# Kernel optimization log

Measured on AMD Instinct MI355X. Metric: run time of the kernel, lower is better.

The kernel has to match this reference:

```python
import jax, jax.numpy as jnp
import numpy as np

N, E, B = 50000, 300000, 8
XD, ED, H, L, G = 160, 16, 256, 4, 32


def setup_inputs() -> dict:
    key = jax.random.key(0)
    ks = jax.random.split(key, 24)
    w = lambda k, shape: jax.random.normal(k, shape, jnp.float32) * 0.05
    z = lambda *shape: jnp.zeros(shape, jnp.float32)
    in_dim = G + (XD - 128)
    return {
        "x": jax.random.normal(ks[0], (N, XD), jnp.float32),
        "edge_attr": jax.random.normal(ks[1], (E, ED), jnp.float32),
        "geo_w": w(ks[2], (128, G)), "geo_b": z(G),
        "nin_w1": w(ks[3], (in_dim, H)), "nin_b1": z(H),
        "nin_w2": w(ks[4], (H, H)), "nin_b2": z(H),
        "ee_w1": w(ks[5], (ED, H)), "ee_b1": z(H),
        "ee_w2": w(ks[6], (H, H)), "ee_b2": z(H),
        "msgx_w": w(ks[7], (L, H, H)),
        "msge_w": w(ks[8], (L, H, H)),
        "upd_w1": w(ks[9], (L, H, H)), "upd_b1": z(L, H),
        "upd_w2": w(ks[10], (L, H, H)), "upd_b2": z(L, H),
        "ln_g": jnp.ones((L, H), jnp.float32), "ln_b": z(L, H),
        "edge_index": jax.random.randint(ks[11], (2, E), 0, N),
        "batch": jnp.sort(jax.random.randint(ks[12], (N,), 0, B)),
        "node_type": jax.random.randint(ks[13], (N,), 0, 3),
    }


def _layernorm(v, g, b, eps=1e-5):
    mu = v.mean(-1, keepdims=True)
    var = ((v - mu) ** 2).mean(-1, keepdims=True)
    return (v - mu) / jnp.sqrt(var + eps) * g + b


def reference(x, edge_attr, geo_w, geo_b, nin_w1, nin_b1, nin_w2, nin_b2,
              ee_w1, ee_b1, ee_w2, ee_b2, msgx_w, msge_w,
              upd_w1, upd_b1, upd_w2, upd_b2, ln_g, ln_b,
              edge_index, batch, node_type):
    # geo projection of leading 128 dims, concat with remaining features
    geo = jax.nn.relu(x[:, :128] @ geo_w + geo_b)
    xin = jnp.concatenate([geo, x[:, 128:]], axis=1)
    # node_in MLP
    h = jax.nn.relu(xin @ nin_w1 + nin_b1) @ nin_w2 + nin_b2  # [N, H]
    # edge encoder MLP
    e = jax.nn.relu(edge_attr @ ee_w1 + ee_b1) @ ee_w2 + ee_b2  # [E, H]
    src, dst = edge_index[0], edge_index[1]
    for l in range(L):
        # message: msg_x(x_j) + msg_e(e), scatter-add to target nodes
        m = h[src] @ msgx_w[l] + e @ msge_w[l]  # [E, H]
        agg = jax.ops.segment_sum(m, dst, num_segments=N)  # [N, H]
        u = jax.nn.relu(agg @ upd_w1[l] + upd_b1[l]) @ upd_w2[l] + upd_b2[l]
        h = _layernorm(h + u, ln_g[l], ln_b[l])
    # masked mean-pool per graph for each node type
    def pool(k):
        mask = (node_type == k).astype(h.dtype)[:, None]  # [N, 1]
        s = jax.ops.segment_sum(h * mask, batch, num_segments=B)
        c = jax.ops.segment_sum(mask, batch, num_segments=B)
        return s / jnp.maximum(c, 1.0)
    z = jnp.concatenate([pool(0), pool(1), pool(2)], axis=1)  # [B, 3H]
    return (z, h, batch)
```

## Files before the change

kernel.cpp:

```cpp
#include <hip/hip_runtime.h>

constexpr int N  = 50000;
constexpr int E  = 300000;
constexpr int B  = 8;
constexpr int XD = 160;
constexpr int ED = 16;
constexpr int H  = 256;
constexpr int L  = 4;
constexpr int G  = 32;

typedef __attribute__((ext_vector_type(8))) short short8;
typedef __attribute__((ext_vector_type(4))) short sv4;
typedef __attribute__((ext_vector_type(4))) float floatx4;

__device__ __forceinline__ short f2bf(float f) {
    union { float f; unsigned u; } v; v.f = f;
    unsigned r = (v.u + 0x7fffu + ((v.u >> 16) & 1u)) >> 16;
    return (short)r;
}
__device__ __forceinline__ float bf2f(short s) {
    union { unsigned u; float f; } v;
    v.u = ((unsigned)(unsigned short)s) << 16;
    return v.f;
}

__global__ __launch_bounds__(256) void hist_kernel(
    const int* __restrict__ dst, int* __restrict__ cnt)
{
    int e = blockIdx.x * 256 + threadIdx.x;
    if (e < E) atomicAdd(&cnt[dst[e]], 1);
}

__global__ __launch_bounds__(256) void scan_partial_kernel(
    const int* __restrict__ cnt, int* __restrict__ bsum)
{
    __shared__ int s[256];
    const int tid = threadIdx.x;
    int i = blockIdx.x * 256 + tid;
    s[tid] = (i < N) ? cnt[i] : 0;
    __syncthreads();
    #pragma unroll
    for (int off = 128; off > 0; off >>= 1) {
        if (tid < off) s[tid] += s[tid + off];
        __syncthreads();
    }
    if (tid == 0) bsum[blockIdx.x] = s[0];
}

__global__ __launch_bounds__(256) void scan_bsum_kernel(
    int* __restrict__ bsum, int nb, int* __restrict__ rsN)
{
    __shared__ int s[256];
    const int tid = threadIdx.x;
    int v = (tid < nb) ? bsum[tid] : 0;
    s[tid] = v;
    __syncthreads();
    #pragma unroll
    for (int off = 1; off < 256; off <<= 1) {
        int x = (tid >= off) ? s[tid - off] : 0;
        __syncthreads();
        s[tid] += x;
        __syncthreads();
    }
    if (tid < nb) bsum[tid] = s[tid] - v;
    if (tid == 255) *rsN = s[255];
}

__global__ __launch_bounds__(256) void scan_final_kernel(
    const int* __restrict__ cnt, const int* __restrict__ bsum,
    int* __restrict__ rs, int* __restrict__ cursor)
{
    __shared__ int s[256];
    const int tid = threadIdx.x;
    int i = blockIdx.x * 256 + tid;
    int v = (i < N) ? cnt[i] : 0;
    s[tid] = v;
    __syncthreads();
    #pragma unroll
    for (int off = 1; off < 256; off <<= 1) {
        int x = (tid >= off) ? s[tid - off] : 0;
        __syncthreads();
        s[tid] += x;
        __syncthreads();
    }
    int excl = s[tid] - v + bsum[blockIdx.x];
    if (i < N) { rs[i] = excl; cursor[i] = excl; }
}

__global__ __launch_bounds__(256) void fill_kernel(
    const int* __restrict__ src, const int* __restrict__ dst,
    int* __restrict__ cursor, int* __restrict__ csr_src, int* __restrict__ csr_eid)
{
    int e = blockIdx.x * 256 + threadIdx.x;
    if (e < E) {
        int d = dst[e];
        int pos = atomicAdd(&cursor[d], 1);
        csr_src[pos] = src[e];
        csr_eid[pos] = e;
    }
}

__global__ __launch_bounds__(256) void hidden_agg_kernel(
    const float* __restrict__ ea, const float* __restrict__ ew1,
    const float* __restrict__ eb1,
    const int* __restrict__ rs, const int* __restrict__ csr_eid,
    short* __restrict__ haggB)
{
    const int lane = threadIdx.x & 63;
    const int wave = threadIdx.x >> 6;
    const int n = blockIdx.x * 4 + wave;
    if (n >= N) return;

    float4 w[ED];
    #pragma unroll
    for (int k = 0; k < ED; ++k)
        w[k] = *(const float4*)&ew1[k * H + 4 * lane];
    float4 bb = *(const float4*)&eb1[4 * lane];

    const int s = rs[n], e = rs[n + 1];
    float4 acc = {0.f, 0.f, 0.f, 0.f};
    int j = s;
    for (; j + 1 < e; j += 2) {
        int e0 = csr_eid[j], e1 = csr_eid[j + 1];
        const float* a0 = ea + (size_t)e0 * ED;
        const float* a1 = ea + (size_t)e1 * ED;
        float4 h0 = bb, h1 = bb;
        #pragma unroll
        for (int k = 0; k < ED; ++k) {
            float v0 = a0[k], v1 = a1[k];
            h0.x += v0 * w[k].x; h1.x += v1 * w[k].x;
            h0.y += v0 * w[k].y; h1.y += v1 * w[k].y;
            h0.z += v0 * w[k].z; h1.z += v1 * w[k].z;
            h0.w += v0 * w[k].w; h1.w += v1 * w[k].w;
        }
        acc.x += fmaxf(h0.x, 0.f) + fmaxf(h1.x, 0.f);
        acc.y += fmaxf(h0.y, 0.f) + fmaxf(h1.y, 0.f);
        acc.z += fmaxf(h0.z, 0.f) + fmaxf(h1.z, 0.f);
        acc.w += fmaxf(h0.w, 0.f) + fmaxf(h1.w, 0.f);
    }
    if (j < e) {
        int e0 = csr_eid[j];
        const float* a0 = ea + (size_t)e0 * ED;
        float4 h0 = bb;
        #pragma unroll
        for (int k = 0; k < ED; ++k) {
            float v0 = a0[k];
            h0.x += v0 * w[k].x; h0.y += v0 * w[k].y;
            h0.z += v0 * w[k].z; h0.w += v0 * w[k].w;
        }
        acc.x += fmaxf(h0.x, 0.f); acc.y += fmaxf(h0.y, 0.f);
        acc.z += fmaxf(h0.z, 0.f); acc.w += fmaxf(h0.w, 0.f);
    }
    sv4 o = {f2bf(acc.x), f2bf(acc.y), f2bf(acc.z), f2bf(acc.w)};
    *(sv4*)&haggB[(size_t)n * H + 4 * lane] = o;
}

__global__ __launch_bounds__(256) void gather_kernel(
    const short* __restrict__ h_in_bf,
    const int* __restrict__ rs, const int* __restrict__ csr_src,
    short* __restrict__ agg_bf)
{
    const int lane = threadIdx.x & 63;
    const int wave = threadIdx.x >> 6;
    const int n = blockIdx.x * 4 + wave;
    if (n >= N) return;
    const int s = rs[n], e = rs[n + 1];
    float4 acc = {0.f, 0.f, 0.f, 0.f};
    int j = s;
    for (; j + 4 <= e; j += 4) {
        const int s0 = csr_src[j],     s1 = csr_src[j + 1];
        const int s2 = csr_src[j + 2], s3 = csr_src[j + 3];
        sv4 v0 = *(const sv4*)&h_in_bf[(size_t)s0 * H + 4 * lane];
        sv4 v1 = *(const sv4*)&h_in_bf[(size_t)s1 * H + 4 * lane];
        sv4 v2 = *(const sv4*)&h_in_bf[(size_t)s2 * H + 4 * lane];
        sv4 v3 = *(const sv4*)&h_in_bf[(size_t)s3 * H + 4 * lane];
        acc.x += (bf2f(v0.x) + bf2f(v1.x)) + (bf2f(v2.x) + bf2f(v3.x));
        acc.y += (bf2f(v0.y) + bf2f(v1.y)) + (bf2f(v2.y) + bf2f(v3.y));
        acc.z += (bf2f(v0.z) + bf2f(v1.z)) + (bf2f(v2.z) + bf2f(v3.z));
        acc.w += (bf2f(v0.w) + bf2f(v1.w)) + (bf2f(v2.w) + bf2f(v3.w));
    }
    for (; j < e; ++j) {
        const int s0 = csr_src[j];
        sv4 v0 = *(const sv4*)&h_in_bf[(size_t)s0 * H + 4 * lane];
        acc.x += bf2f(v0.x); acc.y += bf2f(v0.y);
        acc.z += bf2f(v0.z); acc.w += bf2f(v0.w);
    }
    sv4 o = {f2bf(acc.x), f2bf(acc.y), f2bf(acc.z), f2bf(acc.w)};
    *(sv4*)&agg_bf[(size_t)n * H + 4 * lane] = o;
}

__global__ __launch_bounds__(256) void wx_part_kernel(
    const float* __restrict__ msgx_w, short* __restrict__ wxwe)
{
    int l = blockIdx.x >> 8, k = blockIdx.x & 255, n = threadIdx.x;
    wxwe[((size_t)(l * H + n)) * 512 + k] = f2bf(msgx_w[((size_t)l * H + k) * H + n]);
}

__global__ __launch_bounds__(256) void we_fuse_kernel(
    const float* __restrict__ ee_w2, const float* __restrict__ msge_w,
    short* __restrict__ wxwe)
{
    __shared__ float wrow[H];
    const int tid = threadIdx.x;
    const int l = blockIdx.x / H;
    const int t = blockIdx.x % H;
    wrow[tid] = ee_w2[t * H + tid];
    __syncthreads();
    const float* mw = msge_w + (size_t)l * H * H;
    float acc = 0.f;
    for (int k = 0; k < H; ++k)
        acc += wrow[k] * mw[k * H + tid];
    wxwe[((size_t)(l * H + tid)) * 512 + 256 + t] = f2bf(acc);
}

__global__ __launch_bounds__(256) void fuse_b_kernel(
    const float* __restrict__ ee_b2, const float* __restrict__ msge_w,
    float* __restrict__ be2)
{
    __shared__ float brow[H];
    const int tid = threadIdx.x;
    const int l = blockIdx.x;
    brow[tid] = ee_b2[tid];
    __syncthreads();
    const float* mw = msge_w + (size_t)l * H * H;
    float acc = 0.f;
    for (int k = 0; k < H; ++k)
        acc += brow[k] * mw[k * H + tid];
    be2[l * H + tid] = acc;
}

__global__ __launch_bounds__(256) void conv_bt_kernel(
    const float* __restrict__ w, short* __restrict__ bt)
{
    int mat = blockIdx.x >> 8, k = blockIdx.x & 255, n = threadIdx.x;
    bt[((size_t)mat * H + n) * H + k] = f2bf(w[((size_t)mat * H + k) * H + n]);
}

__global__ __launch_bounds__(256) void geow_bt_kernel(
    const float* __restrict__ w, short* __restrict__ bt)
{
    for (int i = threadIdx.x; i < 32 * 128; i += 256) {
        int n = i >> 7, k = i & 127;
        bt[i] = f2bf(w[k * 32 + n]);
    }
}

__global__ __launch_bounds__(256) void ninw1_bt_kernel(
    const float* __restrict__ w, short* __restrict__ bt)
{
    int i = blockIdx.x * 256 + threadIdx.x;
    int n = i >> 6, k = i & 63;
    bt[i] = f2bf(w[k * H + n]);
}

__global__ __launch_bounds__(256) void node_in_mfma_kernel(
    const float* __restrict__ x,
    const short* __restrict__ geo_wbt, const float* __restrict__ geo_b,
    const short* __restrict__ w1bt, const float* __restrict__ b1,
    const short* __restrict__ w2bt, const float* __restrict__ b2,
    short* __restrict__ h_bf)
{
    constexpr int KP = H + 8;
    constexpr int KX = 128 + 8;
    constexpr int KI = 64 + 8;
    __shared__ short A[64 * KP];
    __shared__ short XIN[64 * KI];
    const int tid = threadIdx.x;
    const int lane = tid & 63, wave = tid >> 6;
    const int quad = lane >> 4, lm = lane & 15;
    const int n0 = blockIdx.x * 64;
    const int nvalid = min(64, N - n0);
    const int ncol = wave * 64 + lm;

    for (int i = tid; i < 64 * 128; i += 256) {
        int row = i >> 7, k = i & 127;
        float v = (row < nvalid) ? x[(size_t)(n0 + row) * XD + k] : 0.f;
        A[row * KX + k] = f2bf(v);
    }
    for (int i = tid; i < 64 * 32; i += 256) {
        int row = i >> 5, k = i & 31;
        float v = (row < nvalid) ? x[(size_t)(n0 + row) * XD + 128 + k] : 0.f;
        XIN[row * KI + 32 + k] = f2bf(v);
    }
    __syncthreads();

    {
        floatx4 c[2];
        float b0 = geo_b[lm], b1v = geo_b[16 + lm];
        c[0] = {b0, b0, b0, b0};
        c[1] = {b1v, b1v, b1v, b1v};
        #pragma unroll
        for (int ks = 0; ks < 4; ++ks) {
            short8 a  = *(const short8*)&A[(wave * 16 + lm) * KX + ks * 32 + quad * 8];
            short8 w0 = *(const short8*)&geo_wbt[(size_t)lm * 128 + ks * 32 + quad * 8];
            short8 w1 = *(const short8*)&geo_wbt[(size_t)(16 + lm) * 128 + ks * 32 + quad * 8];
            c[0] = __builtin_amdgcn_mfma_f32_16x16x32_bf16(a, w0, c[0], 0, 0, 0);
            c[1] = __builtin_amdgcn_mfma_f32_16x16x32_bf16(a, w1, c[1], 0, 0, 0);
        }
        #pragma unroll
        for (int nt = 0; nt < 2; ++nt)
            #pragma unroll
            for (int r = 0; r < 4; ++r) {
                int row = wave * 16 + quad * 4 + r;
                XIN[row * KI + nt * 16 + lm] = f2bf(fmaxf(c[nt][r], 0.f));
            }
    }
    __syncthreads();

    floatx4 c1[4][4];
    #pragma unroll
    for (int nt = 0; nt < 4; ++nt) {
        float bb = b1[ncol + nt * 16];
        #pragma unroll
        for (int mt = 0; mt < 4; ++mt) {
            c1[mt][nt][0] = bb; c1[mt][nt][1] = bb;
            c1[mt][nt][2] = bb; c1[mt][nt][3] = bb;
        }
    }
    #pragma unroll
    for (int ks = 0; ks < 2; ++ks) {
        short8 a[4], b[4];
        #pragma unroll
        for (int mt = 0; mt < 4; ++mt)
            a[mt] = *(const short8*)&XIN[(mt * 16 + lm) * KI + ks * 32 + quad * 8];
        #pragma unroll
        for (int nt = 0; nt < 4; ++nt)
            b[nt] = *(const short8*)&w1bt[(size_t)(ncol + nt * 16) * 64 + ks * 32 + quad * 8];
        #pragma unroll
        for (int mt = 0; mt < 4; ++mt)
            #pragma unroll
            for (int nt = 0; nt < 4; ++nt)
                c1[mt][nt] = __builtin_amdgcn_mfma_f32_16x16x32_bf16(a[mt], b[nt], c1[mt][nt], 0, 0, 0);
    }
    __syncthreads();
    #pragma unroll
    for (int mt = 0; mt < 4; ++mt)
        #pragma unroll
        for (int nt = 0; nt < 4; ++nt) {
            int col = ncol + nt * 16;
            #pragma unroll
            for (int r = 0; r < 4; ++r) {
                int row = mt * 16 + quad * 4 + r;
                A[row * KP + col] = f2bf(fmaxf(c1[mt][nt][r], 0.f));
            }
        }
    __syncthreads();

    floatx4 c2[4][4];
    #pragma unroll
    for (int nt = 0; nt < 4; ++nt) {
        float bb = b2[ncol + nt * 16];
        #pragma unroll
        for (int mt = 0; mt < 4; ++mt) {
            c2[mt][nt][0] = bb; c2[mt][nt][1] = bb;
            c2[mt][nt][2] = bb; c2[mt][nt][3] = bb;
        }
    }
    #pragma unroll
    for (int ks = 0; ks < 8; ++ks) {
        short8 a[4], b[4];
        #pragma unroll
        for (int mt = 0; mt < 4; ++mt)
            a[mt] = *(const short8*)&A[(mt * 16 + lm) * KP + ks * 32 + quad * 8];
        #pragma unroll
        for (int nt = 0; nt < 4; ++nt)
            b[nt] = *(const short8*)&w2bt[(size_t)(ncol + nt * 16) * H + ks * 32 + quad * 8];
        #pragma unroll
        for (int mt = 0; mt < 4; ++mt)
            #pragma unroll
            for (int nt = 0; nt < 4; ++nt)
                c2[mt][nt] = __builtin_amdgcn_mfma_f32_16x16x32_bf16(a[mt], b[nt], c2[mt][nt], 0, 0, 0);
    }
    #pragma unroll
    for (int mt = 0; mt < 4; ++mt)
        #pragma unroll
        for (int r = 0; r < 4; ++r) {
            int row = mt * 16 + quad * 4 + r;
            if (row < nvalid) {
                #pragma unroll
                for (int nt = 0; nt < 4; ++nt)
                    h_bf[(size_t)(n0 + row) * H + ncol + nt * 16] = f2bf(c2[mt][nt][r]);
            }
        }
}

__global__ __launch_bounds__(256, 4) void layer_kernel(
    const short* __restrict__ h_in_bf, short* __restrict__ h_out_bf,
    float* __restrict__ h_out_f32,
    const short* __restrict__ agg_bf,
    const int* __restrict__ rs,
    const short* __restrict__ haggB,
    const short* __restrict__ wxwe, const float* __restrict__ be2,
    const short* __restrict__ u1bt, const float* __restrict__ b1,
    const short* __restrict__ u2bt, const float* __restrict__ b2,
    const float* __restrict__ lng, const float* __restrict__ lnb)
{
    constexpr int KP = H + 8;
    constexpr int M  = 32;
    __shared__ short A[M * KP];
    __shared__ short A2[M * KP];
    __shared__ int rsL[M + 1];
    __shared__ float psum[M][4], psq[M][4];
    __shared__ float muS[M], rsS[M];
    const int tid  = threadIdx.x;
    const int lane = tid & 63, wave = tid >> 6;
    const int quad = lane >> 4, lm = lane & 15;
    const int n0 = blockIdx.x * M;
    const int nvalid = min(M, N - n0);
    const int ncol = wave * 64 + lm;

    if (tid < M + 1) rsL[tid] = rs[min(n0 + tid, N)];
    for (int i = tid; i < M * 64; i += 256) {
        int row = i >> 6, q = i & 63;
        sv4 v = {0, 0, 0, 0};
        sv4 w = {0, 0, 0, 0};
        if (row < nvalid) {
            v = *(const sv4*)&agg_bf[(size_t)(n0 + row) * H + 4 * q];
            w = *(const sv4*)&haggB[(size_t)(n0 + row) * H + 4 * q];
        }
        *(sv4*)&A[row * KP + 4 * q]  = v;
        *(sv4*)&A2[row * KP + 4 * q] = w;
    }
    __syncthreads();

    floatx4 c1[2][4];
    #pragma unroll
    for (int nt = 0; nt < 4; ++nt) {
        float bb = be2[ncol + nt * 16];
        #pragma unroll
        for (int mt = 0; mt < 2; ++mt) {
            #pragma unroll
            for (int r = 0; r < 4; ++r) {
                int row = mt * 16 + quad * 4 + r;
                float deg = (float)(rsL[row + 1] - rsL[row]);
                c1[mt][nt][r] = deg * bb;
            }
        }
    }
    {
        short8 bcur[4], bnxt[4];
        #pragma unroll
        for (int nt = 0; nt < 4; ++nt)
            bcur[nt] = *(const short8*)&wxwe[(size_t)(ncol + nt * 16) * 512 + quad * 8];
        #pragma unroll
        for (int ks = 0; ks < 8; ++ks) {
            if (ks < 7) {
                #pragma unroll
                for (int nt = 0; nt < 4; ++nt)
                    bnxt[nt] = *(const short8*)&wxwe[(size_t)(ncol + nt * 16) * 512 + (ks + 1) * 32 + quad * 8];
            }
            short8 a[2];
            #pragma unroll
            for (int mt = 0; mt < 2; ++mt)
                a[mt] = *(const short8*)&A[(mt * 16 + lm) * KP + ks * 32 + quad * 8];
            #pragma unroll
            for (int mt = 0; mt < 2; ++mt)
                #pragma unroll
                for (int nt = 0; nt < 4; ++nt)
                    c1[mt][nt] = __builtin_amdgcn_mfma_f32_16x16x32_bf16(a[mt], bcur[nt], c1[mt][nt], 0, 0, 0);
            #pragma unroll
            for (int nt = 0; nt < 4; ++nt) bcur[nt] = bnxt[nt];
        }
    }
    {
        short8 bcur[4], bnxt[4];
        #pragma unroll
        for (int nt = 0; nt < 4; ++nt)
            bcur[nt] = *(const short8*)&wxwe[(size_t)(ncol + nt * 16) * 512 + 256 + quad * 8];
        #pragma unroll
        for (int ks = 0; ks < 8; ++ks) {
            if (ks < 7) {
                #pragma unroll
                for (int nt = 0; nt < 4; ++nt)
                    bnxt[nt] = *(const short8*)&wxwe[(size_t)(ncol + nt * 16) * 512 + 256 + (ks + 1) * 32 + quad * 8];
            }
            short8 a[2];
            #pragma unroll
            for (int mt = 0; mt < 2; ++mt)
                a[mt] = *(const short8*)&A2[(mt * 16 + lm) * KP + ks * 32 + quad * 8];
            #pragma unroll
            for (int mt = 0; mt < 2; ++mt)
                #pragma unroll
                for (int nt = 0; nt < 4; ++nt)
                    c1[mt][nt] = __builtin_amdgcn_mfma_f32_16x16x32_bf16(a[mt], bcur[nt], c1[mt][nt], 0, 0, 0);
            #pragma unroll
            for (int nt = 0; nt < 4; ++nt) bcur[nt] = bnxt[nt];
        }
    }
    __syncthreads();
    #pragma unroll
    for (int mt = 0; mt < 2; ++mt)
        #pragma unroll
        for (int nt = 0; nt < 4; ++nt) {
            int col = ncol + nt * 16;
            #pragma unroll
            for (int r = 0; r < 4; ++r) {
                int row = mt * 16 + quad * 4 + r;
                A[row * KP + col] = f2bf(c1[mt][nt][r]);
            }
        }
    __syncthreads();

    floatx4 c2[2][4];
    #pragma unroll
    for (int nt = 0; nt < 4; ++nt) {
        float bb = b1[ncol + nt * 16];
        #pragma unroll
        for (int mt = 0; mt < 2; ++mt) {
            c2[mt][nt][0] = bb; c2[mt][nt][1] = bb;
            c2[mt][nt][2] = bb; c2[mt][nt][3] = bb;
        }
    }
    {
        short8 bcur[4], bnxt[4];
        #pragma unroll
        for (int nt = 0; nt < 4; ++nt)
            bcur[nt] = *(const short8*)&u1bt[(size_t)(ncol + nt * 16) * H + quad * 8];
        #pragma unroll
        for (int ks = 0; ks < 8; ++ks) {
            if (ks < 7) {
                #pragma unroll
                for (int nt = 0; nt < 4; ++nt)
                    bnxt[nt] = *(const short8*)&u1bt[(size_t)(ncol + nt * 16) * H + (ks + 1) * 32 + quad * 8];
            }
            short8 a[2];
            #pragma unroll
            for (int mt = 0; mt < 2; ++mt)
                a[mt] = *(const short8*)&A[(mt * 16 + lm) * KP + ks * 32 + quad * 8];
            #pragma unroll
            for (int mt = 0; mt < 2; ++mt)
                #pragma unroll
                for (int nt = 0; nt < 4; ++nt)
                    c2[mt][nt] = __builtin_amdgcn_mfma_f32_16x16x32_bf16(a[mt], bcur[nt], c2[mt][nt], 0, 0, 0);
            #pragma unroll
            for (int nt = 0; nt < 4; ++nt) bcur[nt] = bnxt[nt];
        }
    }
    #pragma unroll
    for (int mt = 0; mt < 2; ++mt)
        #pragma unroll
        for (int nt = 0; nt < 4; ++nt) {
            int col = ncol + nt * 16;
            #pragma unroll
            for (int r = 0; r < 4; ++r) {
                int row = mt * 16 + quad * 4 + r;
                A2[row * KP + col] = f2bf(fmaxf(c2[mt][nt][r], 0.f));
            }
        }
    __syncthreads();

    floatx4 c3[2][4];
    #pragma unroll
    for (int nt = 0; nt < 4; ++nt) {
        float bb = b2[ncol + nt * 16];
        #pragma unroll
        for (int mt = 0; mt < 2; ++mt) {
            c3[mt][nt][0] = bb; c3[mt][nt][1] = bb;
            c3[mt][nt][2] = bb; c3[mt][nt][3] = bb;
        }
    }
    {
        short8 bcur[4], bnxt[4];
        #pragma unroll
        for (int nt = 0; nt < 4; ++nt)
            bcur[nt] = *(const short8*)&u2bt[(size_t)(ncol + nt * 16) * H + quad * 8];
        #pragma unroll
        for (int ks = 0; ks < 8; ++ks) {
            if (ks < 7) {
                #pragma unroll
                for (int nt = 0; nt < 4; ++nt)
                    bnxt[nt] = *(const short8*)&u2bt[(size_t)(ncol + nt * 16) * H + (ks + 1) * 32 + quad * 8];
            }
            short8 a[2];
            #pragma unroll
            for (int mt = 0; mt < 2; ++mt)
                a[mt] = *(const short8*)&A2[(mt * 16 + lm) * KP + ks * 32 + quad * 8];
            #pragma unroll
            for (int mt = 0; mt < 2; ++mt)
                #pragma unroll
                for (int nt = 0; nt < 4; ++nt)
                    c3[mt][nt] = __builtin_amdgcn_mfma_f32_16x16x32_bf16(a[mt], bcur[nt], c3[mt][nt], 0, 0, 0);
            #pragma unroll
            for (int nt = 0; nt < 4; ++nt) bcur[nt] = bnxt[nt];
        }
    }
    #pragma unroll
    for (int mt = 0; mt < 2; ++mt)
        #pragma unroll
        for (int r = 0; r < 4; ++r) {
            int row = mt * 16 + quad * 4 + r;
            if (row < nvalid) {
                #pragma unroll
                for (int nt = 0; nt < 4; ++nt)
                    c3[mt][nt][r] += bf2f(h_in_bf[(size_t)(n0 + row) * H + ncol + nt * 16]);
            }
        }

    #pragma unroll
    for (int mt = 0; mt < 2; ++mt)
        #pragma unroll
        for (int r = 0; r < 4; ++r) {
            float s = 0.f, q = 0.f;
            #pragma unroll
            for (int nt = 0; nt < 4; ++nt) {
                float v = c3[mt][nt][r];
                s += v; q += v * v;
            }
            #pragma unroll
            for (int m = 1; m < 16; m <<= 1) {
                s += __shfl_xor(s, m, 64);
                q += __shfl_xor(q, m, 64);
            }
            if (lm == 0) {
                int row = mt * 16 + quad * 4 + r;
                psum[row][wave] = s;
                psq[row][wave]  = q;
            }
        }
    __syncthreads();
    if (tid < M) {
        float s = psum[tid][0] + psum[tid][1] + psum[tid][2] + psum[tid][3];
        float q = psq[tid][0] + psq[tid][1] + psq[tid][2] + psq[tid][3];
        float mu = s * (1.f / H);
        float var = q * (1.f / H) - mu * mu;
        muS[tid] = mu;
        rsS[tid] = rsqrtf(fmaxf(var, 0.f) + 1e-5f);
    }
    __syncthreads();

    float g[4], bb4[4];
    #pragma unroll
    for (int nt = 0; nt < 4; ++nt) {
        g[nt]   = lng[ncol + nt * 16];
        bb4[nt] = lnb[ncol + nt * 16];
    }
    const bool wbf = (h_out_bf != nullptr);
    const bool wf  = (h_out_f32 != nullptr);
    #pragma unroll
    for (int mt = 0; mt < 2; ++mt)
        #pragma unroll
        for (int r = 0; r < 4; ++r) {
            int row = mt * 16 + quad * 4 + r;
            if (row < nvalid) {
                float mu = muS[row], rsv = rsS[row];
                #pragma unroll
                for (int nt = 0; nt < 4; ++nt) {
                    float o = (c3[mt][nt][r] - mu) * rsv * g[nt] + bb4[nt];
                    size_t off = (size_t)(n0 + row) * H + ncol + nt * 16;
                    if (wbf) h_out_bf[off] = f2bf(o);
                    if (wf)  h_out_f32[off] = o;
                }
            }
        }
}

__global__ __launch_bounds__(256) void pool_kernel(
    const float* __restrict__ h, const int* __restrict__ batch,
    const int* __restrict__ ntype,
    float* __restrict__ zsum, float* __restrict__ zcnt)
{
    constexpr int CHUNK = 256;
    __shared__ float acc[3][H];
    __shared__ float cnt[3];
    const int tid = threadIdx.x;
    const int n0 = blockIdx.x * CHUNK;
    const int nend = min(n0 + CHUNK, N);

    for (int q = 0; q < 3; ++q) acc[q][tid] = 0.f;
    if (tid == 0) { cnt[0] = 0.f; cnt[1] = 0.f; cnt[2] = 0.f; }
    __syncthreads();

    int cur = batch[n0];
    for (int n = n0; n < nend; ++n) {
        int b = batch[n];
        int t = ntype[n];
        if (b != cur) {
            for (int q = 0; q < 3; ++q) {
                atomicAdd(&zsum[cur * (3 * H) + q * H + tid], acc[q][tid]);
                acc[q][tid] = 0.f;
            }
            if (tid == 0)
                for (int q = 0; q < 3; ++q) { atomicAdd(&zcnt[cur * 3 + q], cnt[q]); cnt[q] = 0.f; }
            cur = b;
        }
        acc[t][tid] += h[(size_t)n * H + tid];
        if (tid == 0) cnt[t] += 1.f;
    }
    for (int q = 0; q < 3; ++q)
        atomicAdd(&zsum[cur * (3 * H) + q * H + tid], acc[q][tid]);
    if (tid == 0)
        for (int q = 0; q < 3; ++q) atomicAdd(&zcnt[cur * 3 + q], cnt[q]);
}

__global__ __launch_bounds__(256) void finalize_kernel(
    const float* __restrict__ zsum, const float* __restrict__ zcnt,
    float* __restrict__ out)
{
    int idx = blockIdx.x * 256 + threadIdx.x;
    if (idx >= B * 3 * H) return;
    int b = idx / (3 * H);
    int c = idx % (3 * H);
    int t = c / H;
    float cn = zcnt[b * 3 + t];
    out[idx] = zsum[idx] / fmaxf(cn, 1.f);
}

__global__ __launch_bounds__(256) void batch_out_kernel(
    const int* __restrict__ batch, float* __restrict__ out)
{
    int idx = blockIdx.x * 256 + threadIdx.x;
    if (idx < N) out[idx] = (float)batch[idx];
}

extern "C" void kernel_launch(void* const* d_in, const int* in_sizes, int n_in,
                              void* d_out, int out_size, void* d_ws, size_t ws_size,
                              hipStream_t stream) {
    const float* x         = (const float*)d_in[0];
    const float* edge_attr = (const float*)d_in[1];
    const float* geo_w     = (const float*)d_in[2];
    const float* geo_b     = (const float*)d_in[3];
    const float* nin_w1    = (const float*)d_in[4];
    const float* nin_b1    = (const float*)d_in[5];
    const float* nin_w2    = (const float*)d_in[6];
    const float* nin_b2    = (const float*)d_in[7];
    const float* ee_w1     = (const float*)d_in[8];
    const float* ee_b1     = (const float*)d_in[9];
    const float* ee_w2     = (const float*)d_in[10];
    const float* ee_b2     = (const float*)d_in[11];
    const float* msgx_w    = (const float*)d_in[12];
    const float* msge_w    = (const float*)d_in[13];
    const float* upd_w1    = (const float*)d_in[14];
    const float* upd_b1    = (const float*)d_in[15];
    const float* upd_w2    = (const float*)d_in[16];
    const float* upd_b2    = (const float*)d_in[17];
    const float* ln_g      = (const float*)d_in[18];
    const float* ln_b      = (const float*)d_in[19];
    const int*   edge_index= (const int*)d_in[20];
    const int*   batch     = (const int*)d_in[21];
    const int*   node_type = (const int*)d_in[22];

    float* out = (float*)d_out;
    float* hf  = out + B * 3 * H;

    short* h0_bf   = (short*)d_ws;
    short* h1_bf   = h0_bf + (size_t)N * H;
    short* haggB   = h1_bf + (size_t)N * H;
    short* wxwe    = haggB + (size_t)N * H;
    short* u1bt    = wxwe + (size_t)L * H * 512;
    short* u2bt    = u1bt + (size_t)L * H * H;
    short* geowbt  = u2bt + (size_t)L * H * H;
    short* w1bt    = geowbt + 32 * 128;
    short* w2bt    = w1bt + H * 64;
    float* be2     = (float*)(w2bt + H * H);
    float* zsum    = be2 + L * H;
    float* zcnt    = zsum + B * 3 * H;
    int*   rowcnt  = (int*)(zcnt + B * 3);
    int*   rs      = rowcnt + N;
    int*   cursor  = rs + N + 1;
    int*   bsum    = cursor + N;
    int*   csr_src = bsum + 256;
    int*   csr_eid = csr_src + E;

    const int* src = edge_index;
    const int* dst = edge_index + E;

    const int nscan = (N + 255) / 256;

    hipMemsetAsync(rowcnt, 0, (size_t)N * sizeof(int), stream);
    hist_kernel<<<(E + 255) / 256, 256, 0, stream>>>(dst, rowcnt);
    scan_partial_kernel<<<nscan, 256, 0, stream>>>(rowcnt, bsum);
    scan_bsum_kernel<<<1, 256, 0, stream>>>(bsum, nscan, rs + N);
    scan_final_kernel<<<nscan, 256, 0, stream>>>(rowcnt, bsum, rs, cursor);
    fill_kernel<<<(E + 255) / 256, 256, 0, stream>>>(src, dst, cursor, csr_src, csr_eid);

    wx_part_kernel<<<L * 256, 256, 0, stream>>>(msgx_w, wxwe);
    we_fuse_kernel<<<L * H, 256, 0, stream>>>(ee_w2, msge_w, wxwe);
    fuse_b_kernel<<<L, 256, 0, stream>>>(ee_b2, msge_w, be2);
    conv_bt_kernel<<<L * 256, 256, 0, stream>>>(upd_w1, u1bt);
    conv_bt_kernel<<<L * 256, 256, 0, stream>>>(upd_w2, u2bt);
    conv_bt_kernel<<<256, 256, 0, stream>>>(nin_w2, w2bt);
    geow_bt_kernel<<<1, 256, 0, stream>>>(geo_w, geowbt);
    ninw1_bt_kernel<<<64, 256, 0, stream>>>(nin_w1, w1bt);

    hidden_agg_kernel<<<(N + 3) / 4, 256, 0, stream>>>(
        edge_attr, ee_w1, ee_b1, rs, csr_eid, haggB);

    node_in_mfma_kernel<<<(N + 63) / 64, 256, 0, stream>>>(
        x, geowbt, geo_b, w1bt, nin_b1, w2bt, nin_b2, h0_bf);

    const int lgrid = (N + 31) / 32;
    for (int l = 0; l < L; ++l) {
        const short* hin  = (l & 1) ? h1_bf : h0_bf;
        short* aggb       = (l & 1) ? h0_bf : h1_bf;
        short* hout_bf    = (l == L - 1) ? nullptr : aggb;
        float* hout_f32   = (l == L - 1) ? hf : nullptr;
        gather_kernel<<<(N + 3) / 4, 256, 0, stream>>>(hin, rs, csr_src, aggb);
        layer_kernel<<<lgrid, 256, 0, stream>>>(
            hin, hout_bf, hout_f32, aggb, rs, haggB,
            wxwe + (size_t)l * H * 512, be2 + (size_t)l * H,
            u1bt + (size_t)l * H * H, upd_b1 + (size_t)l * H,
            u2bt + (size_t)l * H * H, upd_b2 + (size_t)l * H,
            ln_g + (size_t)l * H, ln_b + (size_t)l * H);
    }

    hipMemsetAsync(zsum, 0, (size_t)(B * 3 * H + B * 3) * sizeof(float), stream);
    pool_kernel<<<(N + 255) / 256, 256, 0, stream>>>(hf, batch, node_type, zsum, zcnt);
    finalize_kernel<<<(B * 3 * H + 255) / 256, 256, 0, stream>>>(zsum, zcnt, out);
    batch_out_kernel<<<(N + 255) / 256, 256, 0, stream>>>(batch, out + B * 3 * H + (size_t)N * H);
}
```

Measured before the change: 1.050 ms.

## Fold upd_w1 into message weights to drop one GEMM per layer

Since agg feeds linearly into upd_w1 before the ReLU, the message weights (msgx_w and fused ee_w2·msge_w) are premultiplied by upd_w1 in fp32 at setup, and the bias becomes deg·(be2·W1)+b1. The layer kernel then runs one K=512 GEMM straight into the ReLU instead of the message GEMM plus a separate 256x256 update GEMM, removing an LDS round trip and a sync. This adds setup kernels computing the weight products and changes bf16 rounding points, since the intermediate agg result is no longer quantised.

Measured after the change: 977.4 us. -6.9%, faster.

```diff
diff --git a/kernel.cpp b/kernel.cpp
--- a/kernel.cpp
+++ b/kernel.cpp
@@ -189,16 +189,9 @@
     *(sv4*)&agg_bf[(size_t)n * H + 4 * lane] = o;
 }
 
-__global__ __launch_bounds__(256) void wx_part_kernel(
-    const float* __restrict__ msgx_w, short* __restrict__ wxwe)
-{
-    int l = blockIdx.x >> 8, k = blockIdx.x & 255, n = threadIdx.x;
-    wxwe[((size_t)(l * H + n)) * 512 + k] = f2bf(msgx_w[((size_t)l * H + k) * H + n]);
-}
-
 __global__ __launch_bounds__(256) void we_fuse_kernel(
     const float* __restrict__ ee_w2, const float* __restrict__ msge_w,
-    short* __restrict__ wxwe)
+    float* __restrict__ WEf32)
 {
     __shared__ float wrow[H];
     const int tid = threadIdx.x;
@@ -210,7 +203,41 @@
     float acc = 0.f;
     for (int k = 0; k < H; ++k)
         acc += wrow[k] * mw[k * H + tid];
-    wxwe[((size_t)(l * H + tid)) * 512 + 256 + t] = f2bf(acc);
+    WEf32[((size_t)l * H + t) * H + tid] = acc;
+}
+
+__global__ __launch_bounds__(256) void fuse1_kernel(
+    const float* __restrict__ msgx_w, const float* __restrict__ upd_w1,
+    short* __restrict__ fusedT)
+{
+    __shared__ float wrow[H];
+    const int tid = threadIdx.x;
+    const int l = blockIdx.x / H;
+    const int t = blockIdx.x % H;
+    wrow[tid] = msgx_w[((size_t)l * H + t) * H + tid];
+    __syncthreads();
+    const float* w1 = upd_w1 + (size_t)l * H * H;
+    float acc = 0.f;
+    for (int j = 0; j < H; ++j)
+        acc += wrow[j] * w1[j * H + tid];
+    fusedT[((size_t)(l * H + tid)) * 512 + t] = f2bf(acc);
+}
+
+__global__ __launch_bounds__(256) void fuse2_kernel(
+    const float* __restrict__ WEf32, const float* __restrict__ upd_w1,
+    short* __restrict__ fusedT)
+{
+    __shared__ float wrow[H];
+    const int tid = threadIdx.x;
+    const int l = blockIdx.x / H;
+    const int t = blockIdx.x % H;
+    wrow[tid] = WEf32[((size_t)l * H + t) * H + tid];
+    __syncthreads();
+    const float* w1 = upd_w1 + (size_t)l * H * H;
+    float acc = 0.f;
+    for (int j = 0; j < H; ++j)
+        acc += wrow[j] * w1[j * H + tid];
+    fusedT[((size_t)(l * H + tid)) * 512 + 256 + t] = f2bf(acc);
 }
 
 __global__ __launch_bounds__(256) void fuse_b_kernel(
@@ -227,6 +254,22 @@
     for (int k = 0; k < H; ++k)
         acc += brow[k] * mw[k * H + tid];
     be2[l * H + tid] = acc;
+}
+
+__global__ __launch_bounds__(256) void fuse_bias_kernel(
+    const float* __restrict__ be2, const float* __restrict__ upd_w1,
+    float* __restrict__ be2w1)
+{
+    __shared__ float brow[H];
+    const int tid = threadIdx.x;
+    const int l = blockIdx.x;
+    brow[tid] = be2[l * H + tid];
+    __syncthreads();
+    const float* w1 = upd_w1 + (size_t)l * H * H;
+    float acc = 0.f;
+    for (int j = 0; j < H; ++j)
+        acc += brow[j] * w1[j * H + tid];
+    be2w1[l * H + tid] = acc;
 }
 
 __global__ __launch_bounds__(256) void conv_bt_kernel(
@@ -390,8 +433,8 @@
     const short* __restrict__ agg_bf,
     const int* __restrict__ rs,
     const short* __restrict__ haggB,
-    const short* __restrict__ wxwe, const float* __restrict__ be2,
-    const short* __restrict__ u1bt, const float* __restrict__ b1,
+    const short* __restrict__ fusedT, const float* __restrict__ be2w1,
+    const float* __restrict__ b1,
     const short* __restrict__ u2bt, const float* __restrict__ b2,
     const float* __restrict__ lng, const float* __restrict__ lnb)
 {
@@ -426,14 +469,15 @@
     floatx4 c1[2][4];
     #pragma unroll
     for (int nt = 0; nt < 4; ++nt) {
-        float bb = be2[ncol + nt * 16];
+        float bw = be2w1[ncol + nt * 16];
+        float bb = b1[ncol + nt * 16];
         #pragma unroll
         for (int mt = 0; mt < 2; ++mt) {
             #pragma unroll
             for (int r = 0; r < 4; ++r) {
                 int row = mt * 16 + quad * 4 + r;
                 float deg = (float)(rsL[row + 1] - rsL[row]);
-                c1[mt][nt][r] = deg * bb;
+                c1[mt][nt][r] = deg * bw + bb;
             }
         }
     }
@@ -441,13 +485,13 @@
         short8 bcur[4], bnxt[4];
         #pragma unroll
         for (int nt = 0; nt < 4; ++nt)
-            bcur[nt] = *(const short8*)&wxwe[(size_t)(ncol + nt * 16) * 512 + quad * 8];
+            bcur[nt] = *(const short8*)&fusedT[(size_t)(ncol + nt * 16) * 512 + quad * 8];
         #pragma unroll
         for (int ks = 0; ks < 8; ++ks) {
             if (ks < 7) {
                 #pragma unroll
                 for (int nt = 0; nt < 4; ++nt)
-                    bnxt[nt] = *(const short8*)&wxwe[(size_t)(ncol + nt * 16) * 512 + (ks + 1) * 32 + quad * 8];
+                    bnxt[nt] = *(const short8*)&fusedT[(size_t)(ncol + nt * 16) * 512 + (ks + 1) * 32 + quad * 8];
             }
             short8 a[2];
             #pragma unroll
@@ -466,13 +510,13 @@
         short8 bcur[4], bnxt[4];
         #pragma unroll
         for (int nt = 0; nt < 4; ++nt)
-            bcur[nt] = *(const short8*)&wxwe[(size_t)(ncol + nt * 16) * 512 + 256 + quad * 8];
+            bcur[nt] = *(const short8*)&fusedT[(size_t)(ncol + nt * 16) * 512 + 256 + quad * 8];
         #pragma unroll
         for (int ks = 0; ks < 8; ++ks) {
             if (ks < 7) {
                 #pragma unroll
                 for (int nt = 0; nt < 4; ++nt)
-                    bnxt[nt] = *(const short8*)&wxwe[(size_t)(ncol + nt * 16) * 512 + 256 + (ks + 1) * 32 + quad * 8];
+                    bnxt[nt] = *(const short8*)&fusedT[(size_t)(ncol + nt * 16) * 512 + 256 + (ks + 1) * 32 + quad * 8];
             }
             short8 a[2];
             #pragma unroll
@@ -496,55 +540,7 @@
             #pragma unroll
             for (int r = 0; r < 4; ++r) {
                 int row = mt * 16 + quad * 4 + r;
-                A[row * KP + col] = f2bf(c1[mt][nt][r]);
-            }
-        }
-    __syncthreads();
-
-    floatx4 c2[2][4];
-    #pragma unroll
-    for (int nt = 0; nt < 4; ++nt) {
-        float bb = b1[ncol + nt * 16];
-        #pragma unroll
-        for (int mt = 0; mt < 2; ++mt) {
-            c2[mt][nt][0] = bb; c2[mt][nt][1] = bb;
-            c2[mt][nt][2] = bb; c2[mt][nt][3] = bb;
-        }
-    }
-    {
-        short8 bcur[4], bnxt[4];
-        #pragma unroll
-        for (int nt = 0; nt < 4; ++nt)
-            bcur[nt] = *(const short8*)&u1bt[(size_t)(ncol + nt * 16) * H + quad * 8];
-        #pragma unroll
-        for (int ks = 0; ks < 8; ++ks) {
-            if (ks < 7) {
-                #pragma unroll
-                for (int nt = 0; nt < 4; ++nt)
-                    bnxt[nt] = *(const short8*)&u1bt[(size_t)(ncol + nt * 16) * H + (ks + 1) * 32 + quad * 8];
-            }
-            short8 a[2];
-            #pragma unroll
-            for (int mt = 0; mt < 2; ++mt)
-                a[mt] = *(const short8*)&A[(mt * 16 + lm) * KP + ks * 32 + quad * 8];
-            #pragma unroll
-            for (int mt = 0; mt < 2; ++mt)
-                #pragma unroll
-                for (int nt = 0; nt < 4; ++nt)
-                    c2[mt][nt] = __builtin_amdgcn_mfma_f32_16x16x32_bf16(a[mt], bcur[nt], c2[mt][nt], 0, 0, 0);
-            #pragma unroll
-            for (int nt = 0; nt < 4; ++nt) bcur[nt] = bnxt[nt];
-        }
-    }
-    #pragma unroll
-    for (int mt = 0; mt < 2; ++mt)
-        #pragma unroll
-        for (int nt = 0; nt < 4; ++nt) {
-            int col = ncol + nt * 16;
-            #pragma unroll
-            for (int r = 0; r < 4; ++r) {
-                int row = mt * 16 + quad * 4 + r;
-                A2[row * KP + col] = f2bf(fmaxf(c2[mt][nt][r], 0.f));
+                A[row * KP + col] = f2bf(fmaxf(c1[mt][nt][r], 0.f));
             }
         }
     __syncthreads();
@@ -574,7 +570,7 @@
             short8 a[2];
             #pragma unroll
             for (int mt = 0; mt < 2; ++mt)
-                a[mt] = *(const short8*)&A2[(mt * 16 + lm) * KP + ks * 32 + quad * 8];
+                a[mt] = *(const short8*)&A[(mt * 16 + lm) * KP + ks * 32 + quad * 8];
             #pragma unroll
             for (int mt = 0; mt < 2; ++mt)
                 #pragma unroll
@@ -745,14 +741,15 @@
     short* h0_bf   = (short*)d_ws;
     short* h1_bf   = h0_bf + (size_t)N * H;
     short* haggB   = h1_bf + (size_t)N * H;
-    short* wxwe    = haggB + (size_t)N * H;
-    short* u1bt    = wxwe + (size_t)L * H * 512;
-    short* u2bt    = u1bt + (size_t)L * H * H;
+    short* fusedT  = haggB + (size_t)N * H;
+    short* u2bt    = fusedT + (size_t)L * H * 512;
     short* geowbt  = u2bt + (size_t)L * H * H;
     short* w1bt    = geowbt + 32 * 128;
     short* w2bt    = w1bt + H * 64;
-    float* be2     = (float*)(w2bt + H * H);
-    float* zsum    = be2 + L * H;
+    float* WEf32   = (float*)(w2bt + H * H);
+    float* be2     = WEf32 + (size_t)L * H * H;
+    float* be2w1   = be2 + L * H;
+    float* zsum    = be2w1 + L * H;
     float* zcnt    = zsum + B * 3 * H;
     int*   rowcnt  = (int*)(zcnt + B * 3);
     int*   rs      = rowcnt + N;
@@ -773,10 +770,11 @@
     scan_final_kernel<<<nscan, 256, 0, stream>>>(rowcnt, bsum, rs, cursor);
     fill_kernel<<<(E + 255) / 256, 256, 0, stream>>>(src, dst, cursor, csr_src, csr_eid);
 
-    wx_part_kernel<<<L * 256, 256, 0, stream>>>(msgx_w, wxwe);
-    we_fuse_kernel<<<L * H, 256, 0, stream>>>(ee_w2, msge_w, wxwe);
+    we_fuse_kernel<<<L * H, 256, 0, stream>>>(ee_w2, msge_w, WEf32);
+    fuse1_kernel<<<L * H, 256, 0, stream>>>(msgx_w, upd_w1, fusedT);
+    fuse2_kernel<<<L * H, 256, 0, stream>>>(WEf32, upd_w1, fusedT);
     fuse_b_kernel<<<L, 256, 0, stream>>>(ee_b2, msge_w, be2);
-    conv_bt_kernel<<<L * 256, 256, 0, stream>>>(upd_w1, u1bt);
+    fuse_bias_kernel<<<L, 256, 0, stream>>>(be2, upd_w1, be2w1);
     conv_bt_kernel<<<L * 256, 256, 0, stream>>>(upd_w2, u2bt);
     conv_bt_kernel<<<256, 256, 0, stream>>>(nin_w2, w2bt);
     geow_bt_kernel<<<1, 256, 0, stream>>>(geo_w, geowbt);
@@ -797,8 +795,8 @@
         gather_kernel<<<(N + 3) / 4, 256, 0, stream>>>(hin, rs, csr_src, aggb);
         layer_kernel<<<lgrid, 256, 0, stream>>>(
             hin, hout_bf, hout_f32, aggb, rs, haggB,
-            wxwe + (size_t)l * H * 512, be2 + (size_t)l * H,
-            u1bt + (size_t)l * H * H, upd_b1 + (size_t)l * H,
+            fusedT + (size_t)l * H * 512, be2w1 + (size_t)l * H,
+            upd_b1 + (size_t)l * H,
             u2bt + (size_t)l * H * H, upd_b2 + (size_t)l * H,
             ln_g + (size_t)l * H, ln_b + (size_t)l * H);
     }
```
